# Performance work log

Hardware: AMD Instinct MI355X
Metric: run time of the kernel (lower is better)

The kernel has to match this reference:

```python
import jax, jax.numpy as jnp
import numpy as np

COST_CLASS = 1.0
COST_POLYLINE = 1.0
NUM_QUERIES, BS, NUM_CLASSES = 100, 8, 4
N_PTS, N_TGT = 30, 512


def setup_inputs() -> dict:
    key = jax.random.key(0)
    k1, k2, k3, k4 = jax.random.split(key, 4)
    return {
        "pred_logits": jax.random.normal(k1, (NUM_QUERIES, BS, NUM_CLASSES), dtype=jnp.float32),
        "pred_polylines": jax.random.normal(k2, (NUM_QUERIES, BS, N_PTS, 2), dtype=jnp.float32),
        "tgt_ids": jax.random.randint(k3, (N_TGT,), 0, NUM_CLASSES, dtype=jnp.int32),
        "tgt_polylines": jax.random.normal(k4, (N_TGT, N_PTS, 2), dtype=jnp.float32),
    }


def reference(pred_logits, pred_polylines, tgt_ids, tgt_polylines):
    nq, bs, nc = pred_logits.shape
    # flatten(0,1): [nq*bs, C] / [nq*bs, n_pts, 2]
    out_prob = jax.nn.softmax(pred_logits.reshape(nq * bs, nc), axis=-1)
    out_poly = pred_polylines.reshape(nq * bs, -1, 2)

    # classification cost: -p(target class), [P, T]
    cost_class = -out_prob[:, tgt_ids]

    # pairwise symmetric chamfer with L1 point distance.
    # D[p, t, i, j] = ||out_poly[p, i] - tgt_polylines[t, j]||_1  -> [P, T, np, nt]
    D = jnp.abs(out_poly[:, None, :, None, :] - tgt_polylines[None, :, None, :, :]).sum(-1)
    min1 = D.min(axis=3).mean(axis=2)  # pred -> tgt
    min2 = D.min(axis=2).mean(axis=2)  # tgt -> pred
    cost_polyline = (min1 + min2) * 0.5

    C = COST_CLASS * cost_class + COST_POLYLINE * cost_polyline
    # original does C.view(bs, num_queries, -1) on the (nq, bs)-flattened axis;
    # replicate that exact memory reinterpretation.
    return C.reshape(bs, nq, -1)
```

## Files before the change

kernel.cpp:

```cpp
#include <hip/hip_runtime.h>
#include <math.h>

#define NQ      100
#define BS      8
#define NC      4
#define NPTS    30
#define NTGT    512
#define P_TOTAL (NQ*BS)
#define TILE_P  8
#define TILE_T  32
#define NTHREADS 256

typedef float f32x2 __attribute__((ext_vector_type(2)));

__device__ __forceinline__ f32x2 pksub(f32x2 a, f32x2 b) {
    f32x2 r;
    asm("v_pk_add_f32 %0, %1, %2 neg_lo:[0,1] neg_hi:[0,1]"
        : "=v"(r) : "v"(a), "v"(b));
    return r;
}
__device__ __forceinline__ float maxabs2(f32x2 w) {
    float d;
    asm("v_max_f32 %0, abs(%1), abs(%2)" : "=v"(d) : "v"(w.x), "v"(w.y));
    return d;
}
__device__ __forceinline__ float min3f(float a, float b, float c) {
    float r;
    asm("v_min3_f32 %0, %1, %2, %3" : "=v"(r) : "v"(a), "v"(b), "v"(c));
    return r;
}

__global__ __launch_bounds__(NTHREADS) void matcher_kernel(
    const float* __restrict__ logits,
    const float* __restrict__ pred_poly,
    const int*   __restrict__ tgt_ids,
    const float* __restrict__ tgt_poly,
    float*       __restrict__ out)
{
    __shared__ f32x2 srt_t[NPTS][TILE_T + 1];
    __shared__ f32x2 srt_p[TILE_P][NPTS];
    __shared__ float prob_lds[TILE_P][NC];

    const int tid = threadIdx.x;
    const int p0  = blockIdx.x * TILE_P;
    const int t0  = blockIdx.y * TILE_T;

    for (int idx = tid; idx < TILE_T * NPTS; idx += NTHREADS) {
        const int tt = idx / NPTS;
        const int j  = idx - tt * NPTS;
        const float2 v = *reinterpret_cast<const float2*>(
            tgt_poly + (size_t)(t0 + tt) * (NPTS * 2) + j * 2);
        srt_t[j][tt] = f32x2{v.x + v.y, v.x - v.y};
    }
    for (int idx = tid; idx < TILE_P * NPTS; idx += NTHREADS) {
        const int pp = idx / NPTS;
        const int i  = idx - pp * NPTS;
        const float2 v = *reinterpret_cast<const float2*>(
            pred_poly + (size_t)(p0 + pp) * (NPTS * 2) + i * 2);
        srt_p[pp][i] = f32x2{v.x + v.y, v.x - v.y};
    }
    if (tid < TILE_P) {
        const float* l = logits + (size_t)(p0 + tid) * NC;
        const float a0 = l[0], a1 = l[1], a2 = l[2], a3 = l[3];
        const float m  = fmaxf(fmaxf(a0, a1), fmaxf(a2, a3));
        const float e0 = expf(a0 - m), e1 = expf(a1 - m);
        const float e2 = expf(a2 - m), e3 = expf(a3 - m);
        const float inv = 1.0f / (e0 + e1 + e2 + e3);
        prob_lds[tid][0] = e0 * inv;
        prob_lds[tid][1] = e1 * inv;
        prob_lds[tid][2] = e2 * inv;
        prob_lds[tid][3] = e3 * inv;
    }
    __syncthreads();

    const int tl = tid & (TILE_T - 1);
    const int pl = tid >> 5;

    f32x2 st[NPTS];
#pragma unroll
    for (int j = 0; j < NPTS; ++j) st[j] = srt_t[j][tl];

    float m2[NPTS];
#pragma unroll
    for (int j = 0; j < NPTS; ++j) m2[j] = 1e30f;

    float sum1 = 0.0f;
#pragma unroll 1
    for (int i = 0; i < NPTS; i += 2) {
        const f32x2 pr0 = srt_p[pl][i];
        const f32x2 pr1 = srt_p[pl][i + 1];
        float dmin0 = 1e30f, dmin1 = 1e30f;
#pragma unroll
        for (int j = 0; j < NPTS; j += 2) {
            const float d00 = maxabs2(pksub(pr0, st[j]));
            const float d01 = maxabs2(pksub(pr0, st[j + 1]));
            const float d10 = maxabs2(pksub(pr1, st[j]));
            const float d11 = maxabs2(pksub(pr1, st[j + 1]));
            m2[j]     = min3f(m2[j],     d00, d10);
            m2[j + 1] = min3f(m2[j + 1], d01, d11);
            dmin0     = min3f(dmin0, d00, d01);
            dmin1     = min3f(dmin1, d10, d11);
        }
        sum1 += dmin0;
        sum1 += dmin1;
    }
    float sum2 = 0.0f;
#pragma unroll
    for (int j = 0; j < NPTS; ++j) sum2 += m2[j];

    const int   t   = t0 + tl;
    const int   cls = tgt_ids[t];
    const float cc  = -prob_lds[pl][cls];
    out[(size_t)(p0 + pl) * NTGT + t] = cc + (sum1 + sum2) * (0.5f / (float)NPTS);
}

extern "C" void kernel_launch(void* const* d_in, const int* in_sizes, int n_in,
                              void* d_out, int out_size, void* d_ws, size_t ws_size,
                              hipStream_t stream) {
    const float* logits    = (const float*)d_in[0];
    const float* pred_poly = (const float*)d_in[1];
    const int*   tids      = (const int*)d_in[2];
    const float* tgt_poly  = (const float*)d_in[3];
    float*       out       = (float*)d_out;

    dim3 grid(P_TOTAL / TILE_P, NTGT / TILE_T);
    dim3 block(NTHREADS);
    matcher_kernel<<<grid, block, 0, stream>>>(logits, pred_poly, tids, tgt_poly, out);
}
```

Before: 43.47 us.

## Split target points across lane pairs and halve pred tile per block

```diff
diff --git a/kernel.cpp b/kernel.cpp
--- a/kernel.cpp
+++ b/kernel.cpp
@@ -5,9 +5,10 @@
 #define BS      8
 #define NC      4
 #define NPTS    30
+#define J_HALF  15
 #define NTGT    512
 #define P_TOTAL (NQ*BS)
-#define TILE_P  8
+#define TILE_P  4
 #define TILE_T  32
 #define NTHREADS 256
 
@@ -52,9 +53,9 @@
             tgt_poly + (size_t)(t0 + tt) * (NPTS * 2) + j * 2);
         srt_t[j][tt] = f32x2{v.x + v.y, v.x - v.y};
     }
-    for (int idx = tid; idx < TILE_P * NPTS; idx += NTHREADS) {
-        const int pp = idx / NPTS;
-        const int i  = idx - pp * NPTS;
+    if (tid < TILE_P * NPTS) {
+        const int pp = tid / NPTS;
+        const int i  = tid - pp * NPTS;
         const float2 v = *reinterpret_cast<const float2*>(
             pred_poly + (size_t)(p0 + pp) * (NPTS * 2) + i * 2);
         srt_p[pp][i] = f32x2{v.x + v.y, v.x - v.y};
@@ -73,45 +74,62 @@
     }
     __syncthreads();
 
-    const int tl = tid & (TILE_T - 1);
-    const int pl = tid >> 5;
+    const int w     = tid >> 6;
+    const int lane  = tid & 63;
+    const int tl    = lane >> 1;
+    const int jbase = (lane & 1) * J_HALF;
 
-    f32x2 st[NPTS];
+    f32x2 st[J_HALF];
 #pragma unroll
-    for (int j = 0; j < NPTS; ++j) st[j] = srt_t[j][tl];
+    for (int k = 0; k < J_HALF; ++k) {
+        st[k] = srt_t[jbase + k][tl];
+        asm volatile("" : "+v"(st[k]));
+    }
 
-    float m2[NPTS];
+    float m2[J_HALF];
 #pragma unroll
-    for (int j = 0; j < NPTS; ++j) m2[j] = 1e30f;
+    for (int k = 0; k < J_HALF; ++k) m2[k] = 1e30f;
 
     float sum1 = 0.0f;
 #pragma unroll 1
     for (int i = 0; i < NPTS; i += 2) {
-        const f32x2 pr0 = srt_p[pl][i];
-        const f32x2 pr1 = srt_p[pl][i + 1];
+        const f32x2 pr0 = srt_p[w][i];
+        const f32x2 pr1 = srt_p[w][i + 1];
         float dmin0 = 1e30f, dmin1 = 1e30f;
 #pragma unroll
-        for (int j = 0; j < NPTS; j += 2) {
-            const float d00 = maxabs2(pksub(pr0, st[j]));
-            const float d01 = maxabs2(pksub(pr0, st[j + 1]));
-            const float d10 = maxabs2(pksub(pr1, st[j]));
-            const float d11 = maxabs2(pksub(pr1, st[j + 1]));
-            m2[j]     = min3f(m2[j],     d00, d10);
-            m2[j + 1] = min3f(m2[j + 1], d01, d11);
-            dmin0     = min3f(dmin0, d00, d01);
-            dmin1     = min3f(dmin1, d10, d11);
+        for (int k = 0; k < J_HALF - 1; k += 2) {
+            const float d0a = maxabs2(pksub(pr0, st[k]));
+            const float d0b = maxabs2(pksub(pr0, st[k + 1]));
+            const float d1a = maxabs2(pksub(pr1, st[k]));
+            const float d1b = maxabs2(pksub(pr1, st[k + 1]));
+            m2[k]     = min3f(m2[k],     d0a, d1a);
+            m2[k + 1] = min3f(m2[k + 1], d0b, d1b);
+            dmin0     = min3f(dmin0, d0a, d0b);
+            dmin1     = min3f(dmin1, d1a, d1b);
         }
-        sum1 += dmin0;
-        sum1 += dmin1;
+        {
+            const float d0 = maxabs2(pksub(pr0, st[J_HALF - 1]));
+            const float d1 = maxabs2(pksub(pr1, st[J_HALF - 1]));
+            m2[J_HALF - 1] = min3f(m2[J_HALF - 1], d0, d1);
+            dmin0 = fminf(dmin0, d0);
+            dmin1 = fminf(dmin1, d1);
+        }
+        dmin0 = fminf(dmin0, __shfl_xor(dmin0, 1, 64));
+        dmin1 = fminf(dmin1, __shfl_xor(dmin1, 1, 64));
+        sum1 += dmin0 + dmin1;
     }
+
     float sum2 = 0.0f;
 #pragma unroll
-    for (int j = 0; j < NPTS; ++j) sum2 += m2[j];
+    for (int k = 0; k < J_HALF; ++k) sum2 += m2[k];
+    sum2 += __shfl_xor(sum2, 1, 64);
 
-    const int   t   = t0 + tl;
-    const int   cls = tgt_ids[t];
-    const float cc  = -prob_lds[pl][cls];
-    out[(size_t)(p0 + pl) * NTGT + t] = cc + (sum1 + sum2) * (0.5f / (float)NPTS);
+    if ((lane & 1) == 0) {
+        const int   t   = t0 + tl;
+        const int   cls = tgt_ids[t];
+        const float cc  = -prob_lds[w][cls];
+        out[(size_t)(p0 + w) * NTGT + t] = cc + (sum1 + sum2) * (0.5f / (float)NPTS);
+    }
 }
 
 extern "C" void kernel_launch(void* const* d_in, const int* in_sizes, int n_in,
```

New measurement: 45.84 us. 1.05x slower.

## Hold per-wave prediction points in scalar registers and stream targets from LDS

Applied to the files above, without the earlier changes.

```diff
diff --git a/kernel.cpp b/kernel.cpp
--- a/kernel.cpp
+++ b/kernel.cpp
@@ -8,15 +8,16 @@
 #define NTGT    512
 #define P_TOTAL (NQ*BS)
 #define TILE_P  8
-#define TILE_T  32
-#define NTHREADS 256
+#define TILE_T  64
+#define NTHREADS 512
 
-typedef float f32x2 __attribute__((ext_vector_type(2)));
+typedef float        f32x2 __attribute__((ext_vector_type(2)));
+typedef unsigned int u32x2 __attribute__((ext_vector_type(2)));
 
-__device__ __forceinline__ f32x2 pksub(f32x2 a, f32x2 b) {
+__device__ __forceinline__ f32x2 pksub_sv(u32x2 sp, f32x2 t) {
     f32x2 r;
     asm("v_pk_add_f32 %0, %1, %2 neg_lo:[0,1] neg_hi:[0,1]"
-        : "=v"(r) : "v"(a), "v"(b));
+        : "=v"(r) : "s"(sp), "v"(t));
     return r;
 }
 __device__ __forceinline__ float maxabs2(f32x2 w) {
@@ -38,7 +39,6 @@
     float*       __restrict__ out)
 {
     __shared__ f32x2 srt_t[NPTS][TILE_T + 1];
-    __shared__ f32x2 srt_p[TILE_P][NPTS];
     __shared__ float prob_lds[TILE_P][NC];
 
     const int tid = threadIdx.x;
@@ -52,13 +52,6 @@
             tgt_poly + (size_t)(t0 + tt) * (NPTS * 2) + j * 2);
         srt_t[j][tt] = f32x2{v.x + v.y, v.x - v.y};
     }
-    for (int idx = tid; idx < TILE_P * NPTS; idx += NTHREADS) {
-        const int pp = idx / NPTS;
-        const int i  = idx - pp * NPTS;
-        const float2 v = *reinterpret_cast<const float2*>(
-            pred_poly + (size_t)(p0 + pp) * (NPTS * 2) + i * 2);
-        srt_p[pp][i] = f32x2{v.x + v.y, v.x - v.y};
-    }
     if (tid < TILE_P) {
         const float* l = logits + (size_t)(p0 + tid) * NC;
         const float a0 = l[0], a1 = l[1], a2 = l[2], a3 = l[3];
@@ -71,47 +64,55 @@
         prob_lds[tid][2] = e2 * inv;
         prob_lds[tid][3] = e3 * inv;
     }
+
+    const int w  = tid >> 6;
+    const int tl = tid & 63;
+
+    u32x2 sp[NPTS];
+    {
+        const float2* pp = reinterpret_cast<const float2*>(
+            pred_poly + (size_t)(p0 + w) * (NPTS * 2));
+#pragma unroll
+        for (int i = 0; i < NPTS; ++i) {
+            const float2 v = pp[i];
+            sp[i].x = __builtin_amdgcn_readfirstlane(__float_as_uint(v.x + v.y));
+            sp[i].y = __builtin_amdgcn_readfirstlane(__float_as_uint(v.x - v.y));
+        }
+    }
     __syncthreads();
 
-    const int tl = tid & (TILE_T - 1);
-    const int pl = tid >> 5;
+    float m1[NPTS];
+#pragma unroll
+    for (int i = 0; i < NPTS; ++i) m1[i] = 1e30f;
 
-    f32x2 st[NPTS];
+    float sum2 = 0.0f;
+#pragma unroll 1
+    for (int j2 = 0; j2 < NPTS / 2; ++j2) {
+        const f32x2 tv0 = srt_t[2 * j2][tl];
+        const f32x2 tv1 = srt_t[2 * j2 + 1][tl];
+        float dj0 = 1e30f, dj1 = 1e30f;
 #pragma unroll
-    for (int j = 0; j < NPTS; ++j) st[j] = srt_t[j][tl];
-
-    float m2[NPTS];
-#pragma unroll
-    for (int j = 0; j < NPTS; ++j) m2[j] = 1e30f;
+        for (int i = 0; i < NPTS; i += 2) {
+            const float d00 = maxabs2(pksub_sv(sp[i],     tv0));
+            const float d01 = maxabs2(pksub_sv(sp[i],     tv1));
+            const float d10 = maxabs2(pksub_sv(sp[i + 1], tv0));
+            const float d11 = maxabs2(pksub_sv(sp[i + 1], tv1));
+            m1[i]     = min3f(m1[i],     d00, d01);
+            m1[i + 1] = min3f(m1[i + 1], d10, d11);
+            dj0       = min3f(dj0, d00, d10);
+            dj1       = min3f(dj1, d01, d11);
+        }
+        sum2 += dj0 + dj1;
+    }
 
     float sum1 = 0.0f;
-#pragma unroll 1
-    for (int i = 0; i < NPTS; i += 2) {
-        const f32x2 pr0 = srt_p[pl][i];
-        const f32x2 pr1 = srt_p[pl][i + 1];
-        float dmin0 = 1e30f, dmin1 = 1e30f;
 #pragma unroll
-        for (int j = 0; j < NPTS; j += 2) {
-            const float d00 = maxabs2(pksub(pr0, st[j]));
-            const float d01 = maxabs2(pksub(pr0, st[j + 1]));
-            const float d10 = maxabs2(pksub(pr1, st[j]));
-            const float d11 = maxabs2(pksub(pr1, st[j + 1]));
-            m2[j]     = min3f(m2[j],     d00, d10);
-            m2[j + 1] = min3f(m2[j + 1], d01, d11);
-            dmin0     = min3f(dmin0, d00, d01);
-            dmin1     = min3f(dmin1, d10, d11);
-        }
-        sum1 += dmin0;
-        sum1 += dmin1;
-    }
-    float sum2 = 0.0f;
-#pragma unroll
-    for (int j = 0; j < NPTS; ++j) sum2 += m2[j];
+    for (int i = 0; i < NPTS; ++i) sum1 += m1[i];
 
     const int   t   = t0 + tl;
     const int   cls = tgt_ids[t];
-    const float cc  = -prob_lds[pl][cls];
-    out[(size_t)(p0 + pl) * NTGT + t] = cc + (sum1 + sum2) * (0.5f / (float)NPTS);
+    const float cc  = -prob_lds[w][cls];
+    out[(size_t)(p0 + w) * NTGT + t] = cc + (sum1 + sum2) * (0.5f / (float)NPTS);
 }
 
 extern "C" void kernel_launch(void* const* d_in, const int* in_sizes, int n_in,
```

After: 49.01 us. +12.7%, slower.
